# Kernel tuning notes

Measured on AMD Instinct MI355X. Metric: run time of the kernel, lower is better.

Reference implementation:

```python
import jax, jax.numpy as jnp
import numpy as np

N_STATIC, N_DYNAMIC = 64, 32
INPUT_DIM = N_STATIC + N_DYNAMIC * 9 + 8   # 360
EMBED = 64
HIDDEN = 2048
OUT = 512
T = 4096
L_IN0 = INPUT_DIM + EMBED                   # 424


def setup_inputs() -> dict:
    key = jax.random.key(0)
    ks = jax.random.split(key, 11)
    s = lambda k, shape: jax.random.normal(k, shape, jnp.float32) * 0.02
    return {
        "inputVecs": jax.random.normal(ks[0], (T, INPUT_DIM), jnp.float32),
        "Wih0": s(ks[1], (4 * HIDDEN, L_IN0)),
        "bih0": s(ks[2], (4 * HIDDEN,)),
        "bhh0": s(ks[3], (4 * HIDDEN,)),
        "Wih1": s(ks[4], (4 * HIDDEN, HIDDEN)),
        "bih1": s(ks[5], (4 * HIDDEN,)),
        "bhh1": s(ks[6], (4 * HIDDEN,)),
        "Wlin": s(ks[7], (OUT, HIDDEN)),
        "blin": s(ks[8], (OUT,)),
        "Wmap": s(ks[9], (EMBED, OUT)),
        "bmap": s(ks[10], (EMBED,)),
        "embed0": jnp.zeros((EMBED,), jnp.float32),
    }


def _cell(gates):
    # PyTorch LSTM gate order: input, forget, cell(g), output.
    # h0 = c0 = 0 each step -> c = sigmoid(i)*tanh(g), h = sigmoid(o)*tanh(c).
    i, f, g, o = jnp.split(gates, 4)
    c = jax.nn.sigmoid(i) * jnp.tanh(g)
    return jax.nn.sigmoid(o) * jnp.tanh(c)


def reference(inputVecs, Wih0, bih0, bhh0, Wih1, bih1, bhh1, Wlin, blin, Wmap, bmap, embed0):
    # The original calls nn.LSTM without hx every timestep, so PyTorch uses
    # zero initial (h, c): all W_hh @ h terms vanish; only b_hh biases remain.
    # The sole cross-time recurrence is the embed feedback loop.
    D = inputVecs.shape[1]
    Wx, We = Wih0[:, :D], Wih0[:, D:]
    # Hoist the large input GEMM out of the scan: (T, 4H)
    gates_x = inputVecs @ Wx.T + (bih0 + bhh0)
    b1 = bih1 + bhh1

    def step(embed, gx):
        h0 = _cell(gx + We @ embed)              # LSTM layer 0 (single step)
        h1 = _cell(Wih1 @ h0 + b1)               # LSTM layer 1 (single step)
        y = Wlin @ h1 + blin                     # (OUT,)  == linear(lstm_out)
        new_embed = Wmap @ jax.nn.log_softmax(y) + bmap  # map(log_softmax(y))
        return new_embed, y

    _, ys = jax.lax.scan(step, embed0, gates_x)
    return ys                                     # (T, OUT) stacked outputs
```

## Files before the change

### kernel.cpp

```cpp
#include <hip/hip_runtime.h>

#define GWG 256
#define BTH 768
#define WROW 2052
#define LDSZ 137600
#define TB   0x5AB00001

typedef float f4v __attribute__((ext_vector_type(4)));

__device__ __forceinline__ unsigned short b16(float f) {
  union { float f; unsigned int i; } z; z.f = f;
  unsigned int r = z.i + 0x7fffu + ((z.i >> 16) & 1u);
  return (unsigned short)(r >> 16);
}
__device__ __forceinline__ float bup(unsigned short u) {
  union { unsigned int i; float f; } z; z.i = ((unsigned int)u) << 16; return z.f;
}
__device__ __forceinline__ float blo(unsigned int p) {
  union { unsigned int i; float f; } z; z.i = p << 16; return z.f;
}
__device__ __forceinline__ float bhi(unsigned int p) {
  union { unsigned int i; float f; } z; z.i = p & 0xffff0000u; return z.f;
}
__device__ __forceinline__ float sigm(float x) { return 1.f / (1.f + expf(-x)); }

__device__ __forceinline__ void stG(float* p2, f4v v) {
  asm volatile("global_store_dwordx4 %0, %1, off sc0 sc1" :: "v"(p2), "v"(v) : "memory");
}

__device__ __forceinline__ void pollH(const float* mb, int tag, unsigned short* lHb) {
  const int L = threadIdx.x;
  const float* base = mb + L * 4;
  f4v v[8];
  for (;;) {
#pragma unroll
    for (int s = 0; s < 8; ++s)
      asm volatile("global_load_dwordx4 %0, %1, off sc0 sc1"
                   : "=v"(v[s]) : "v"(base + s * 256) : "memory");
    asm volatile("s_waitcnt vmcnt(0)" ::: "memory");
    __builtin_amdgcn_sched_barrier(0);
    bool ok = true;
#pragma unroll
    for (int s = 0; s < 8; ++s) ok &= (__float_as_int(v[s][3]) == tag);
    if (__all(ok)) break;
    __builtin_amdgcn_s_sleep(1);
  }
#pragma unroll
  for (int s = 0; s < 8; ++s) {
    int c = s * 64 + L;
    uint2 u; u.x = __float_as_uint(v[s][0]); u.y = __float_as_uint(v[s][1]);
    *(uint2*)&lHb[c * 4] = u;
  }
}
__device__ __forceinline__ void pollY(const float* mb, int tag, float* lY) {
  const int L = threadIdx.x;
  const float* base = mb + L * 4;
  f4v v[4];
  for (;;) {
#pragma unroll
    for (int s = 0; s < 4; ++s)
      asm volatile("global_load_dwordx4 %0, %1, off sc0 sc1"
                   : "=v"(v[s]) : "v"(base + s * 256) : "memory");
    asm volatile("s_waitcnt vmcnt(0)" ::: "memory");
    __builtin_amdgcn_sched_barrier(0);
    bool ok = true;
#pragma unroll
    for (int s = 0; s < 4; ++s) ok &= (__float_as_int(v[s][3]) == tag);
    if (__all(ok)) break;
    __builtin_amdgcn_s_sleep(1);
  }
#pragma unroll
  for (int s = 0; s < 4; ++s) {
    int c = s * 64 + L;
    lY[c * 2] = v[s][0]; lY[c * 2 + 1] = v[s][1];
  }
}

__global__ __launch_bounds__(256) void prep(const float* __restrict__ bih0, const float* __restrict__ bhh0,
                                            const float* __restrict__ bih1, const float* __restrict__ bhh1,
                                            float* __restrict__ b0, float* __restrict__ b1f) {
  int i = blockIdx.x * 256 + threadIdx.x;
  if (i < 8192) { b0[i] = bih0[i] + bhh0[i]; b1f[i] = bih1[i] + bhh1[i]; }
}

__global__ __launch_bounds__(256) void transpose_wx(const float* __restrict__ Wih0, float* __restrict__ WxT) {
  int idx = blockIdx.x * 256 + threadIdx.x;
  int r = idx & 8191, k = idx >> 13;
  WxT[(size_t)k * 8192 + r] = Wih0[(size_t)r * 424 + k];
}

__global__ __launch_bounds__(256) void gemm_gx(const float* __restrict__ inV, const float* __restrict__ WxT,
                                               const float* __restrict__ b0, unsigned short* __restrict__ gxb) {
  __shared__ float lin[32 * 360];
  int t0 = blockIdx.x * 32;
  int by = blockIdx.y;
  int ry = by >> 3;
  int gatey = ry + (ry ? 1 : 0);
  int r = gatey * 2048 + (by & 7) * 256 + threadIdx.x;
  for (int i = threadIdx.x; i < 32 * 360; i += 256) lin[i] = inV[(size_t)t0 * 360 + i];
  __syncthreads();
  float b = b0[r];
  float acc[32];
#pragma unroll
  for (int tt = 0; tt < 32; ++tt) acc[tt] = b;
  for (int k = 0; k < 360; k += 4) {
    float w0 = WxT[(size_t)(k + 0) * 8192 + r];
    float w1 = WxT[(size_t)(k + 1) * 8192 + r];
    float w2 = WxT[(size_t)(k + 2) * 8192 + r];
    float w3 = WxT[(size_t)(k + 3) * 8192 + r];
#pragma unroll
    for (int tt = 0; tt < 32; ++tt) {
      float4 l = *reinterpret_cast<const float4*>(&lin[tt * 360 + k]);
      acc[tt] = fmaf(w0, l.x, fmaf(w1, l.y, fmaf(w2, l.z, fmaf(w3, l.w, acc[tt]))));
    }
  }
  for (int tt = 0; tt < 32; ++tt) gxb[(size_t)(t0 + tt) * 8192 + r] = b16(acc[tt]);
}

__global__ __launch_bounds__(256) void wcomb_k(const float* __restrict__ Wih0, const float* __restrict__ Wmap,
                                               unsigned short* __restrict__ wcomb) {
  __shared__ float lwe[64];
  int cr = blockIdx.x;
  int orig = cr + (cr >= 2048 ? 2048 : 0);
  if (threadIdx.x < 64) lwe[threadIdx.x] = Wih0[(size_t)orig * 424 + 360 + threadIdx.x];
  __syncthreads();
  int c = threadIdx.x;
  float a0 = 0.f, a1 = 0.f;
  for (int e = 0; e < 64; ++e) {
    float w = lwe[e];
    a0 = fmaf(w, Wmap[e * 512 + c], a0);
    a1 = fmaf(w, Wmap[e * 512 + c + 256], a1);
  }
  wcomb[(size_t)cr * 512 + c] = b16(a0);
  wcomb[(size_t)cr * 512 + c + 256] = b16(a1);
}

__global__ __launch_bounds__(256) void rsk(const unsigned short* __restrict__ wcomb,
                                           const float* __restrict__ Wih0,
                                           const float* __restrict__ bmap, const float* __restrict__ emb0,
                                           float* __restrict__ rs, float* __restrict__ bcomb,
                                           float* __restrict__ g0c) {
  int cr = blockIdx.x * 256 + threadIdx.x;
  if (cr >= 6144) return;
  int orig = cr + (cr >= 2048 ? 2048 : 0);
  float s = 0.f;
  for (int k = 0; k < 512; ++k) s += bup(wcomb[(size_t)cr * 512 + k]);
  float bc = 0.f, g0 = 0.f;
  for (int e = 0; e < 64; ++e) {
    float w = Wih0[(size_t)orig * 424 + 360 + e];
    bc = fmaf(w, bmap[e], bc);
    g0 = fmaf(w, emb0[e], g0);
  }
  rs[cr] = s; bcomb[cr] = bc; g0c[cr] = g0;
}

struct KP {
  const float* Wih1; const float* Wlin; const float* blin; const float* b1f;
  const unsigned short* gxb; const unsigned short* wcomb;
  const float* rs; const float* bcomb; const float* g0c;
  float* mb_h0; float* mb_h1; float* mb_y;
  float* out;
};

__global__ __launch_bounds__(BTH) void lstm_seq(KP p) {
  extern __shared__ __align__(16) char smem[];
  unsigned short* lW1  = (unsigned short*)smem;
  unsigned short* lWcb = (unsigned short*)(smem + 98496);
  unsigned short* lWl  = (unsigned short*)(smem + 123072);
  unsigned short* lHb  = (unsigned short*)(smem + 131264);
  float* lY = (float*)(smem + 135360);
  float* lR = (float*)(smem + 137408);
  float* lV = (float*)(smem + 137504);

  const int w = blockIdx.x, tid = threadIdx.x;
  const int rl = tid >> 5;
  const int l32 = tid & 31;
  const int g3 = rl >> 3;
  const int gate = g3 + (g3 ? 1 : 0);
  const int gr  = w * 8 + (rl & 7) + 2048 * gate;
  const int crt = w * 8 + (rl & 7) + 2048 * g3;

  for (int r2 = 0; r2 < 24; ++r2) {
    int gg = r2 >> 3; int grr = w * 8 + (r2 & 7) + 2048 * (gg + (gg ? 1 : 0));
    const float* src = p.Wih1 + (size_t)grr * 2048;
    for (int i = tid; i < 2048; i += BTH) lW1[r2 * WROW + i] = b16(src[i]);
  }
  for (int i = tid; i < 24 * 512; i += BTH) {
    int r2 = i >> 9, k = i & 511;
    int crr = w * 8 + (r2 & 7) + 2048 * (r2 >> 3);
    lWcb[r2 * 512 + k] = p.wcomb[(size_t)crr * 512 + k];
  }
  for (int i = tid; i < 2 * 2048; i += BTH) {
    int q = i >> 11, k = i & 2047;
    lWl[i] = b16(p.Wlin[(size_t)(w * 2 + q) * 2048 + k]);
  }
  const float b1r = p.b1f[gr];
  const float rs_r = p.rs[crt], bc_r = p.bcomb[crt], g0_r = p.g0c[crt];
  const float bl0 = p.blin[w * 2], bl1 = p.blin[w * 2 + 1];
  unsigned short gxu = p.gxb[gr];
  __syncthreads();

  for (int t = 0; t < 4096; ++t) {
    const int tagt = TB + t;
    const unsigned short gxu_n = p.gxb[(size_t)(t < 4095 ? t + 1 : t) * 8192 + gr];
    if (t > 0) {
      if (tid < 64) pollY(p.mb_y, tagt - 1, lY);
      __syncthreads();
      float s = 0.f;
      if (tid < 512) {
        s = expf(lY[tid]);
#pragma unroll
        for (int d = 1; d < 64; d <<= 1) s += __shfl_xor(s, d);
        if ((tid & 63) == 0) lV[tid >> 6] = s;
      }
      __syncthreads();
      float lse = logf(lV[0] + lV[1] + lV[2] + lV[3] + lV[4] + lV[5] + lV[6] + lV[7]);
      float acc = 0.f;
#pragma unroll
      for (int j = 0; j < 8; ++j) {
        int k = 2 * l32 + 64 * j;
        unsigned uwp = *(const unsigned*)&lWcb[rl * 512 + k];
        float2 yv2 = *(const float2*)&lY[k];
        acc = fmaf(blo(uwp), yv2.x, fmaf(bhi(uwp), yv2.y, acc));
      }
      acc += __shfl_xor(acc, 1); acc += __shfl_xor(acc, 2); acc += __shfl_xor(acc, 4);
      acc += __shfl_xor(acc, 8); acc += __shfl_xor(acc, 16);
      if (l32 == 0) lR[rl] = bup(gxu) + acc - lse * rs_r + bc_r;
    } else {
      if (l32 == 0) lR[rl] = bup(gxu) + g0_r;
    }
    __syncthreads();
    if (tid < 8) {
      float cc = sigm(lR[tid]) * tanhf(lR[8 + tid]);
      float h  = sigm(lR[16 + tid]) * tanhf(cc);
      unsigned hb = (unsigned)b16(h);
      unsigned a0 = __shfl(hb, tid * 4 + 0);
      unsigned a1 = __shfl(hb, tid * 4 + 1);
      unsigned a2 = __shfl(hb, tid * 4 + 2);
      unsigned a3 = __shfl(hb, tid * 4 + 3);
      if (tid < 2) {
        f4v c;
        c[0] = __uint_as_float(a0 | (a1 << 16));
        c[1] = __uint_as_float(a2 | (a3 << 16));
        c[2] = 0.f; c[3] = __int_as_float(tagt);
        stG(p.mb_h0 + w * 8 + tid * 4, c);
      }
    }
    if (tid < 64) pollH(p.mb_h0, tagt, lHb);
    __syncthreads();
    {
      float acc = 0.f;
      const unsigned short* wr = lW1 + rl * WROW;
#pragma unroll 4
      for (int mm = 0; mm < 16; ++mm) {
        int k = l32 * 4 + mm * 128;
        ushort4 uw = *(const ushort4*)&wr[k];
        ushort4 uh = *(const ushort4*)&lHb[k];
        acc = fmaf(bup(uw.x), bup(uh.x), acc);
        acc = fmaf(bup(uw.y), bup(uh.y), acc);
        acc = fmaf(bup(uw.z), bup(uh.z), acc);
        acc = fmaf(bup(uw.w), bup(uh.w), acc);
      }
      acc += __shfl_xor(acc, 1); acc += __shfl_xor(acc, 2); acc += __shfl_xor(acc, 4);
      acc += __shfl_xor(acc, 8); acc += __shfl_xor(acc, 16);
      if (l32 == 0) lR[rl] = acc + b1r;
    }
    __syncthreads();
    if (tid < 8) {
      float cc = sigm(lR[tid]) * tanhf(lR[8 + tid]);
      float h  = sigm(lR[16 + tid]) * tanhf(cc);
      unsigned hb = (unsigned)b16(h);
      unsigned a0 = __shfl(hb, tid * 4 + 0);
      unsigned a1 = __shfl(hb, tid * 4 + 1);
      unsigned a2 = __shfl(hb, tid * 4 + 2);
      unsigned a3 = __shfl(hb, tid * 4 + 3);
      if (tid < 2) {
        f4v c;
        c[0] = __uint_as_float(a0 | (a1 << 16));
        c[1] = __uint_as_float(a2 | (a3 << 16));
        c[2] = 0.f; c[3] = __int_as_float(tagt);
        stG(p.mb_h1 + w * 8 + tid * 4, c);
      }
    }
    if (tid < 64) pollH(p.mb_h1, tagt, lHb);
    __syncthreads();
    if (tid < 512) {
      int q = tid >> 8, l = tid & 255;
      float a = 0.f;
#pragma unroll
      for (int it = 0; it < 2; ++it) {
        int k = it * 1024 + l * 4;
        ushort4 uw = *(const ushort4*)&lWl[q * 2048 + k];
        ushort4 uh = *(const ushort4*)&lHb[k];
        a = fmaf(bup(uw.x), bup(uh.x), a);
        a = fmaf(bup(uw.y), bup(uh.y), a);
        a = fmaf(bup(uw.z), bup(uh.z), a);
        a = fmaf(bup(uw.w), bup(uh.w), a);
      }
#pragma unroll
      for (int d = 1; d < 64; d <<= 1) a += __shfl_xor(a, d);
      if ((tid & 63) == 0) lV[tid >> 6] = a;
    }
    __syncthreads();
    if (tid == 0) {
      float y0 = lV[0] + lV[1] + lV[2] + lV[3] + bl0;
      float y1 = lV[4] + lV[5] + lV[6] + lV[7] + bl1;
      f4v c; c[0] = y0; c[1] = y1; c[2] = 0.f; c[3] = __int_as_float(tagt);
      stG(p.mb_y + w * 4, c);
      p.out[(size_t)t * 512 + w * 2]     = y0;
      p.out[(size_t)t * 512 + w * 2 + 1] = y1;
    }
    gxu = gxu_n;
  }
}

extern "C" void kernel_launch(void* const* d_in, const int* in_sizes, int n_in,
                              void* d_out, int out_size, void* d_ws, size_t ws_size,
                              hipStream_t stream) {
  const float* inV  = (const float*)d_in[0];
  const float* Wih0 = (const float*)d_in[1];
  const float* bih0 = (const float*)d_in[2];
  const float* bhh0 = (const float*)d_in[3];
  const float* Wih1 = (const float*)d_in[4];
  const float* bih1 = (const float*)d_in[5];
  const float* bhh1 = (const float*)d_in[6];
  const float* Wlin = (const float*)d_in[7];
  const float* blin = (const float*)d_in[8];
  const float* Wmap = (const float*)d_in[9];
  const float* bmap = (const float*)d_in[10];
  const float* emb0 = (const float*)d_in[11];

  char* ws = (char*)d_ws;
  unsigned short* gxb   = (unsigned short*)(ws);
  float*          WxT   = (float*)(ws + 67108864);
  unsigned short* wcomb = (unsigned short*)(ws + 67108864);
  float* b0     = (float*)(ws + 78905344);
  float* b1f    = (float*)(ws + 78938112);
  float* mb_h0  = (float*)(ws + 78970880);
  float* mb_h1  = (float*)(ws + 78979072);
  float* mb_y   = (float*)(ws + 78987264);
  float* rs     = (float*)(ws + 78991360);
  float* bcomb  = (float*)(ws + 79015936);
  float* g0c    = (float*)(ws + 79040512);
  float* out    = (float*)d_out;

  prep<<<32, 256, 0, stream>>>(bih0, bhh0, bih1, bhh1, b0, b1f);
  transpose_wx<<<11520, 256, 0, stream>>>(Wih0, WxT);
  gemm_gx<<<dim3(128, 24), 256, 0, stream>>>(inV, WxT, b0, gxb);
  wcomb_k<<<6144, 256, 0, stream>>>(Wih0, Wmap, wcomb);
  rsk<<<24, 256, 0, stream>>>(wcomb, Wih0, bmap, emb0, rs, bcomb, g0c);

  hipFuncSetAttribute(reinterpret_cast<const void*>(lstm_seq),
                      hipFuncAttributeMaxDynamicSharedMemorySize, LDSZ);
  KP p{Wih1, Wlin, blin, b1f, gxb, wcomb, rs, bcomb, g0c, mb_h0, mb_h1, mb_y, out};
  void* args[] = { (void*)&p };
  hipError_t e = hipLaunchCooperativeKernel(reinterpret_cast<void*>(&lstm_seq),
                                            dim3(GWG), dim3(BTH), args, LDSZ, stream);
  if (e != hipSuccess) {
    lstm_seq<<<GWG, BTH, LDSZ, stream>>>(p);
  }
}
```

Measured before the change: 31.46 ms.

## Fold Wmap·Wlin into layer-0 embed weights and exchange only exp-sums

Precomputes We·Wmap·Wlin (6144x2048, bf16) so the embed feedback can be computed directly from the previous h1 instead of from gathered y. Each block now publishes only the sum of exp(y) for its two outputs, so the per-step poll shrinks to a scalar log-sum-exp reduction. The h1·Wbig dot product no longer waits on the y exchange, which shortens the critical path of each step. In exchange each block reads 24 bf16 rows of 2048 from global memory every step rather than 512-wide rows from LDS. The gx buffer is also reduced to the three gates that are actually used.

```diff
diff --git a/kernel.cpp b/kernel.cpp
--- a/kernel.cpp
+++ b/kernel.cpp
@@ -3,7 +3,7 @@
 #define GWG 256
 #define BTH 768
 #define WROW 2052
-#define LDSZ 137600
+#define LDSZ 111296
 #define TB   0x5AB00001
 
 typedef float f4v __attribute__((ext_vector_type(4)));
@@ -52,7 +52,7 @@
     *(uint2*)&lHb[c * 4] = u;
   }
 }
-__device__ __forceinline__ void pollY(const float* mb, int tag, float* lY) {
+__device__ __forceinline__ void pollE(const float* mb, int tag, float* lseSlot) {
   const int L = threadIdx.x;
   const float* base = mb + L * 4;
   f4v v[4];
@@ -69,11 +69,10 @@
     if (__all(ok)) break;
     __builtin_amdgcn_s_sleep(1);
   }
-#pragma unroll
-  for (int s = 0; s < 4; ++s) {
-    int c = s * 64 + L;
-    lY[c * 2] = v[s][0]; lY[c * 2 + 1] = v[s][1];
-  }
+  float s = v[0][0] + v[1][0] + v[2][0] + v[3][0];
+#pragma unroll
+  for (int d = 1; d < 64; d <<= 1) s += __shfl_xor(s, d);
+  if (L == 0) *lseSlot = logf(s);
 }
 
 __global__ __launch_bounds__(256) void prep(const float* __restrict__ bih0, const float* __restrict__ bhh0,
@@ -96,7 +95,8 @@
   int by = blockIdx.y;
   int ry = by >> 3;
   int gatey = ry + (ry ? 1 : 0);
-  int r = gatey * 2048 + (by & 7) * 256 + threadIdx.x;
+  int r  = gatey * 2048 + (by & 7) * 256 + threadIdx.x;
+  int cr = ry    * 2048 + (by & 7) * 256 + threadIdx.x;
   for (int i = threadIdx.x; i < 32 * 360; i += 256) lin[i] = inV[(size_t)t0 * 360 + i];
   __syncthreads();
   float b = b0[r];
@@ -114,63 +114,90 @@
       acc[tt] = fmaf(w0, l.x, fmaf(w1, l.y, fmaf(w2, l.z, fmaf(w3, l.w, acc[tt]))));
     }
   }
-  for (int tt = 0; tt < 32; ++tt) gxb[(size_t)(t0 + tt) * 8192 + r] = b16(acc[tt]);
-}
-
-__global__ __launch_bounds__(256) void wcomb_k(const float* __restrict__ Wih0, const float* __restrict__ Wmap,
-                                               unsigned short* __restrict__ wcomb) {
-  __shared__ float lwe[64];
-  int cr = blockIdx.x;
-  int orig = cr + (cr >= 2048 ? 2048 : 0);
-  if (threadIdx.x < 64) lwe[threadIdx.x] = Wih0[(size_t)orig * 424 + 360 + threadIdx.x];
-  __syncthreads();
-  int c = threadIdx.x;
-  float a0 = 0.f, a1 = 0.f;
-  for (int e = 0; e < 64; ++e) {
-    float w = lwe[e];
-    a0 = fmaf(w, Wmap[e * 512 + c], a0);
-    a1 = fmaf(w, Wmap[e * 512 + c + 256], a1);
-  }
-  wcomb[(size_t)cr * 512 + c] = b16(a0);
-  wcomb[(size_t)cr * 512 + c + 256] = b16(a1);
-}
-
-__global__ __launch_bounds__(256) void rsk(const unsigned short* __restrict__ wcomb,
-                                           const float* __restrict__ Wih0,
-                                           const float* __restrict__ bmap, const float* __restrict__ emb0,
-                                           float* __restrict__ rs, float* __restrict__ bcomb,
+  for (int tt = 0; tt < 32; ++tt) gxb[(size_t)(t0 + tt) * 6144 + cr] = b16(acc[tt]);
+}
+
+__global__ __launch_bounds__(256) void wml_k(const float* __restrict__ Wmap, const float* __restrict__ Wlin,
+                                             float* __restrict__ wml) {
+  __shared__ float lm[512];
+  int e = blockIdx.x;
+  int k = blockIdx.y * 256 + threadIdx.x;
+  for (int i = threadIdx.x; i < 512; i += 256) lm[i] = Wmap[e * 512 + i];
+  __syncthreads();
+  float acc = 0.f;
+  for (int c = 0; c < 512; ++c) acc = fmaf(lm[c], Wlin[(size_t)c * 2048 + k], acc);
+  wml[(size_t)e * 2048 + k] = acc;
+}
+
+__global__ __launch_bounds__(256) void wbig_k(const float* __restrict__ Wih0, const float* __restrict__ wml,
+                                              unsigned short* __restrict__ wbig) {
+  __shared__ float lWe[32 * 64];
+  int cr0 = blockIdx.x * 32;
+  int c = blockIdx.y * 256 + threadIdx.x;
+  for (int i = threadIdx.x; i < 32 * 64; i += 256) {
+    int r2 = i >> 6, e = i & 63;
+    int cr = cr0 + r2; int orig = cr + (cr >= 2048 ? 2048 : 0);
+    lWe[i] = Wih0[(size_t)orig * 424 + 360 + e];
+  }
+  __syncthreads();
+  float wr[64];
+#pragma unroll
+  for (int e = 0; e < 64; ++e) wr[e] = wml[(size_t)e * 2048 + c];
+  for (int r2 = 0; r2 < 32; ++r2) {
+    float acc = 0.f;
+#pragma unroll
+    for (int e = 0; e < 64; ++e) acc = fmaf(lWe[r2 * 64 + e], wr[e], acc);
+    wbig[(size_t)(cr0 + r2) * 2048 + c] = b16(acc);
+  }
+}
+
+__global__ __launch_bounds__(256) void rsk(const float* __restrict__ Wih0, const float* __restrict__ Wmap,
+                                           const float* __restrict__ blin, const float* __restrict__ bmap,
+                                           const float* __restrict__ emb0,
+                                           float* __restrict__ rs, float* __restrict__ bc2,
                                            float* __restrict__ g0c) {
+  __shared__ float mrs[64], mu1[64];
+  if (threadIdx.x < 64) {
+    int e = threadIdx.x;
+    float s = 0.f, u = 0.f;
+    for (int c = 0; c < 512; ++c) {
+      float wv = Wmap[e * 512 + c];
+      s += wv; u = fmaf(wv, blin[c], u);
+    }
+    mrs[e] = s; mu1[e] = u + bmap[e];
+  }
+  __syncthreads();
   int cr = blockIdx.x * 256 + threadIdx.x;
   if (cr >= 6144) return;
   int orig = cr + (cr >= 2048 ? 2048 : 0);
-  float s = 0.f;
-  for (int k = 0; k < 512; ++k) s += bup(wcomb[(size_t)cr * 512 + k]);
-  float bc = 0.f, g0 = 0.f;
+  float a = 0.f, b = 0.f, g = 0.f;
   for (int e = 0; e < 64; ++e) {
     float w = Wih0[(size_t)orig * 424 + 360 + e];
-    bc = fmaf(w, bmap[e], bc);
-    g0 = fmaf(w, emb0[e], g0);
-  }
-  rs[cr] = s; bcomb[cr] = bc; g0c[cr] = g0;
+    a = fmaf(w, mrs[e], a);
+    b = fmaf(w, mu1[e], b);
+    g = fmaf(w, emb0[e], g);
+  }
+  rs[cr] = a; bc2[cr] = b; g0c[cr] = g;
 }
 
 struct KP {
   const float* Wih1; const float* Wlin; const float* blin; const float* b1f;
-  const unsigned short* gxb; const unsigned short* wcomb;
-  const float* rs; const float* bcomb; const float* g0c;
-  float* mb_h0; float* mb_h1; float* mb_y;
+  const unsigned short* gxb; const unsigned short* wbig;
+  const float* rs; const float* bc2; const float* g0c;
+  float* mb_h0; float* mb_h1; float* mb_e;
   float* out;
 };
 
 __global__ __launch_bounds__(BTH) void lstm_seq(KP p) {
   extern __shared__ __align__(16) char smem[];
-  unsigned short* lW1  = (unsigned short*)smem;
-  unsigned short* lWcb = (unsigned short*)(smem + 98496);
-  unsigned short* lWl  = (unsigned short*)(smem + 123072);
-  unsigned short* lHb  = (unsigned short*)(smem + 131264);
-  float* lY = (float*)(smem + 135360);
-  float* lR = (float*)(smem + 137408);
-  float* lV = (float*)(smem + 137504);
+  unsigned short* lW1 = (unsigned short*)smem;
+  unsigned short* lWl = (unsigned short*)(smem + 98496);
+  unsigned short* lHb = (unsigned short*)(smem + 106688);
+  float* lRA = (float*)(smem + 110784);
+  float* lRS = (float*)(smem + 110912);
+  float* lR  = (float*)(smem + 111040);
+  float* lV  = (float*)(smem + 111168);
+  float* lSe = (float*)(smem + 111232);
 
   const int w = blockIdx.x, tid = threadIdx.x;
   const int rl = tid >> 5;
@@ -185,54 +212,49 @@
     const float* src = p.Wih1 + (size_t)grr * 2048;
     for (int i = tid; i < 2048; i += BTH) lW1[r2 * WROW + i] = b16(src[i]);
   }
-  for (int i = tid; i < 24 * 512; i += BTH) {
-    int r2 = i >> 9, k = i & 511;
-    int crr = w * 8 + (r2 & 7) + 2048 * (r2 >> 3);
-    lWcb[r2 * 512 + k] = p.wcomb[(size_t)crr * 512 + k];
-  }
   for (int i = tid; i < 2 * 2048; i += BTH) {
     int q = i >> 11, k = i & 2047;
     lWl[i] = b16(p.Wlin[(size_t)(w * 2 + q) * 2048 + k]);
   }
-  const float b1r = p.b1f[gr];
-  const float rs_r = p.rs[crt], bc_r = p.bcomb[crt], g0_r = p.g0c[crt];
+  const float b1r  = p.b1f[gr];
+  const float rs_r = p.rs[crt], bc2_r = p.bc2[crt], g0_r = p.g0c[crt];
   const float bl0 = p.blin[w * 2], bl1 = p.blin[w * 2 + 1];
-  unsigned short gxu = p.gxb[gr];
+  unsigned short gxu = p.gxb[crt];
+  if (l32 == 0) lRS[rl] = rs_r;
+  const unsigned short* wbr = p.wbig + (size_t)crt * 2048;
   __syncthreads();
 
   for (int t = 0; t < 4096; ++t) {
     const int tagt = TB + t;
-    const unsigned short gxu_n = p.gxb[(size_t)(t < 4095 ? t + 1 : t) * 8192 + gr];
+    const unsigned short gxu_n = p.gxb[(size_t)(t < 4095 ? t + 1 : t) * 6144 + crt];
     if (t > 0) {
-      if (tid < 64) pollY(p.mb_y, tagt - 1, lY);
-      __syncthreads();
-      float s = 0.f;
-      if (tid < 512) {
-        s = expf(lY[tid]);
-#pragma unroll
-        for (int d = 1; d < 64; d <<= 1) s += __shfl_xor(s, d);
-        if ((tid & 63) == 0) lV[tid >> 6] = s;
-      }
-      __syncthreads();
-      float lse = logf(lV[0] + lV[1] + lV[2] + lV[3] + lV[4] + lV[5] + lV[6] + lV[7]);
       float acc = 0.f;
-#pragma unroll
-      for (int j = 0; j < 8; ++j) {
-        int k = 2 * l32 + 64 * j;
-        unsigned uwp = *(const unsigned*)&lWcb[rl * 512 + k];
-        float2 yv2 = *(const float2*)&lY[k];
-        acc = fmaf(blo(uwp), yv2.x, fmaf(bhi(uwp), yv2.y, acc));
+#pragma unroll 4
+      for (int mm = 0; mm < 16; ++mm) {
+        int k = l32 * 4 + mm * 128;
+        ushort4 uw = *(const ushort4*)&wbr[k];
+        ushort4 uh = *(const ushort4*)&lHb[k];
+        acc = fmaf(bup(uw.x), bup(uh.x), acc);
+        acc = fmaf(bup(uw.y), bup(uh.y), acc);
+        acc = fmaf(bup(uw.z), bup(uh.z), acc);
+        acc = fmaf(bup(uw.w), bup(uh.w), acc);
       }
       acc += __shfl_xor(acc, 1); acc += __shfl_xor(acc, 2); acc += __shfl_xor(acc, 4);
       acc += __shfl_xor(acc, 8); acc += __shfl_xor(acc, 16);
-      if (l32 == 0) lR[rl] = bup(gxu) + acc - lse * rs_r + bc_r;
+      if (l32 == 0) lRA[rl] = acc + bup(gxu) + bc2_r;
+      if (tid < 64) pollE(p.mb_e, tagt - 1, lSe);
     } else {
-      if (l32 == 0) lR[rl] = bup(gxu) + g0_r;
+      if (l32 == 0) lRA[rl] = bup(gxu) + g0_r;
+      if (tid == 0) lSe[0] = 0.f;
     }
     __syncthreads();
     if (tid < 8) {
-      float cc = sigm(lR[tid]) * tanhf(lR[8 + tid]);
-      float h  = sigm(lR[16 + tid]) * tanhf(cc);
+      float ls = lSe[0];
+      float pi = lRA[tid]      - ls * lRS[tid];
+      float pg = lRA[8 + tid]  - ls * lRS[8 + tid];
+      float po = lRA[16 + tid] - ls * lRS[16 + tid];
+      float cc = sigm(pi) * tanhf(pg);
+      float h  = sigm(po) * tanhf(cc);
       unsigned hb = (unsigned)b16(h);
       unsigned a0 = __shfl(hb, tid * 4 + 0);
       unsigned a1 = __shfl(hb, tid * 4 + 1);
@@ -305,10 +327,10 @@
     if (tid == 0) {
       float y0 = lV[0] + lV[1] + lV[2] + lV[3] + bl0;
       float y1 = lV[4] + lV[5] + lV[6] + lV[7] + bl1;
-      f4v c; c[0] = y0; c[1] = y1; c[2] = 0.f; c[3] = __int_as_float(tagt);
-      stG(p.mb_y + w * 4, c);
       p.out[(size_t)t * 512 + w * 2]     = y0;
       p.out[(size_t)t * 512 + w * 2 + 1] = y1;
+      f4v c; c[0] = expf(y0) + expf(y1); c[1] = 0.f; c[2] = 0.f; c[3] = __int_as_float(tagt);
+      stG(p.mb_e + w * 4, c);
     }
     gxu = gxu_n;
   }
@@ -331,28 +353,30 @@
   const float* emb0 = (const float*)d_in[11];
 
   char* ws = (char*)d_ws;
-  unsigned short* gxb   = (unsigned short*)(ws);
-  float*          WxT   = (float*)(ws + 67108864);
-  unsigned short* wcomb = (unsigned short*)(ws + 67108864);
-  float* b0     = (float*)(ws + 78905344);
-  float* b1f    = (float*)(ws + 78938112);
-  float* mb_h0  = (float*)(ws + 78970880);
-  float* mb_h1  = (float*)(ws + 78979072);
-  float* mb_y   = (float*)(ws + 78987264);
-  float* rs     = (float*)(ws + 78991360);
-  float* bcomb  = (float*)(ws + 79015936);
-  float* g0c    = (float*)(ws + 79040512);
-  float* out    = (float*)d_out;
+  unsigned short* gxb  = (unsigned short*)(ws);
+  float*          WxT  = (float*)(ws + 50331648);
+  unsigned short* wbig = (unsigned short*)(ws + 50331648);
+  float* wml   = (float*)(ws + 75497472);
+  float* b0    = (float*)(ws + 76021760);
+  float* b1f   = (float*)(ws + 76054528);
+  float* mb_h0 = (float*)(ws + 76087296);
+  float* mb_h1 = (float*)(ws + 76095488);
+  float* mb_e  = (float*)(ws + 76103680);
+  float* rs    = (float*)(ws + 76107776);
+  float* bc2   = (float*)(ws + 76132352);
+  float* g0c   = (float*)(ws + 76156928);
+  float* out   = (float*)d_out;
 
   prep<<<32, 256, 0, stream>>>(bih0, bhh0, bih1, bhh1, b0, b1f);
   transpose_wx<<<11520, 256, 0, stream>>>(Wih0, WxT);
   gemm_gx<<<dim3(128, 24), 256, 0, stream>>>(inV, WxT, b0, gxb);
-  wcomb_k<<<6144, 256, 0, stream>>>(Wih0, Wmap, wcomb);
-  rsk<<<24, 256, 0, stream>>>(wcomb, Wih0, bmap, emb0, rs, bcomb, g0c);
+  wml_k<<<dim3(64, 8), 256, 0, stream>>>(Wmap, Wlin, wml);
+  wbig_k<<<dim3(192, 8), 256, 0, stream>>>(Wih0, wml, wbig);
+  rsk<<<24, 256, 0, stream>>>(Wih0, Wmap, blin, bmap, emb0, rs, bc2, g0c);
 
   hipFuncSetAttribute(reinterpret_cast<const void*>(lstm_seq),
                       hipFuncAttributeMaxDynamicSharedMemorySize, LDSZ);
-  KP p{Wih1, Wlin, blin, b1f, gxb, wcomb, rs, bcomb, g0c, mb_h0, mb_h1, mb_y, out};
+  KP p{Wih1, Wlin, blin, b1f, gxb, wbig, rs, bc2, g0c, mb_h0, mb_h1, mb_e, out};
   void* args[] = { (void*)&p };
   hipError_t e = hipLaunchCooperativeKernel(reinterpret_cast<void*>(&lstm_seq),
                                             dim3(GWG), dim3(BTH), args, LDSZ, stream);
```

New measurement: 33.79 ms. 1.07x slower.

## Replicate mailbox buffers eightfold and overlap log-sum-exp with embed matvec

Applied to the files above, without the earlier changes.

Each workgroup now writes its h0, h1 and y mailbox entries to 8 replicas, and readers poll only the replica picked by blockIdx mod 8. This spreads the polling traffic of 256 workgroups over more cache lines to cut contention on the cross-workgroup sync. The log-sum-exp is now computed by a single wave from its own registers, so one barrier goes away. The lse correction is applied after the gate reduction, which lets the embed matvec run without waiting for it. The gx buffer is also compacted to only the 3 gates used, which shrinks its stride and workspace.

```diff
diff --git a/kernel.cpp b/kernel.cpp
--- a/kernel.cpp
+++ b/kernel.cpp
@@ -3,7 +3,7 @@
 #define GWG 256
 #define BTH 768
 #define WROW 2052
-#define LDSZ 137600
+#define LDSZ 137856
 #define TB   0x5AB00001
 
 typedef float f4v __attribute__((ext_vector_type(4)));
@@ -50,29 +50,6 @@
     int c = s * 64 + L;
     uint2 u; u.x = __float_as_uint(v[s][0]); u.y = __float_as_uint(v[s][1]);
     *(uint2*)&lHb[c * 4] = u;
-  }
-}
-__device__ __forceinline__ void pollY(const float* mb, int tag, float* lY) {
-  const int L = threadIdx.x;
-  const float* base = mb + L * 4;
-  f4v v[4];
-  for (;;) {
-#pragma unroll
-    for (int s = 0; s < 4; ++s)
-      asm volatile("global_load_dwordx4 %0, %1, off sc0 sc1"
-                   : "=v"(v[s]) : "v"(base + s * 256) : "memory");
-    asm volatile("s_waitcnt vmcnt(0)" ::: "memory");
-    __builtin_amdgcn_sched_barrier(0);
-    bool ok = true;
-#pragma unroll
-    for (int s = 0; s < 4; ++s) ok &= (__float_as_int(v[s][3]) == tag);
-    if (__all(ok)) break;
-    __builtin_amdgcn_s_sleep(1);
-  }
-#pragma unroll
-  for (int s = 0; s < 4; ++s) {
-    int c = s * 64 + L;
-    lY[c * 2] = v[s][0]; lY[c * 2 + 1] = v[s][1];
   }
 }
 
@@ -96,7 +73,8 @@
   int by = blockIdx.y;
   int ry = by >> 3;
   int gatey = ry + (ry ? 1 : 0);
-  int r = gatey * 2048 + (by & 7) * 256 + threadIdx.x;
+  int r  = gatey * 2048 + (by & 7) * 256 + threadIdx.x;
+  int cr = ry    * 2048 + (by & 7) * 256 + threadIdx.x;
   for (int i = threadIdx.x; i < 32 * 360; i += 256) lin[i] = inV[(size_t)t0 * 360 + i];
   __syncthreads();
   float b = b0[r];
@@ -114,7 +92,7 @@
       acc[tt] = fmaf(w0, l.x, fmaf(w1, l.y, fmaf(w2, l.z, fmaf(w3, l.w, acc[tt]))));
     }
   }
-  for (int tt = 0; tt < 32; ++tt) gxb[(size_t)(t0 + tt) * 8192 + r] = b16(acc[tt]);
+  for (int tt = 0; tt < 32; ++tt) gxb[(size_t)(t0 + tt) * 6144 + cr] = b16(acc[tt]);
 }
 
 __global__ __launch_bounds__(256) void wcomb_k(const float* __restrict__ Wih0, const float* __restrict__ Wmap,
@@ -165,12 +143,14 @@
 __global__ __launch_bounds__(BTH) void lstm_seq(KP p) {
   extern __shared__ __align__(16) char smem[];
   unsigned short* lW1  = (unsigned short*)smem;
-  unsigned short* lWcb = (unsigned short*)(smem + 98496);
-  unsigned short* lWl  = (unsigned short*)(smem + 123072);
+  unsigned short* lWl  = (unsigned short*)(smem + 98496);
+  unsigned short* lWcb = (unsigned short*)(smem + 106688);
   unsigned short* lHb  = (unsigned short*)(smem + 131264);
-  float* lY = (float*)(smem + 135360);
-  float* lR = (float*)(smem + 137408);
-  float* lV = (float*)(smem + 137504);
+  float* lY  = (float*)(smem + 135360);
+  float* lRA = (float*)(smem + 137408);
+  float* lRS = (float*)(smem + 137536);
+  float* lR  = (float*)(smem + 137664);
+  float* lV  = (float*)(smem + 137792);
 
   const int w = blockIdx.x, tid = threadIdx.x;
   const int rl = tid >> 5;
@@ -179,6 +159,7 @@
   const int gate = g3 + (g3 ? 1 : 0);
   const int gr  = w * 8 + (rl & 7) + 2048 * gate;
   const int crt = w * 8 + (rl & 7) + 2048 * g3;
+  const int rep = w & 7;
 
   for (int r2 = 0; r2 < 24; ++r2) {
     int gg = r2 >> 3; int grr = w * 8 + (r2 & 7) + 2048 * (gg + (gg ? 1 : 0));
@@ -194,27 +175,49 @@
     int q = i >> 11, k = i & 2047;
     lWl[i] = b16(p.Wlin[(size_t)(w * 2 + q) * 2048 + k]);
   }
-  const float b1r = p.b1f[gr];
+  const float b1r  = p.b1f[gr];
   const float rs_r = p.rs[crt], bc_r = p.bcomb[crt], g0_r = p.g0c[crt];
   const float bl0 = p.blin[w * 2], bl1 = p.blin[w * 2 + 1];
-  unsigned short gxu = p.gxb[gr];
+  unsigned short gxu = p.gxb[crt];
+  if (l32 == 0) lRS[rl] = rs_r;
   __syncthreads();
 
   for (int t = 0; t < 4096; ++t) {
     const int tagt = TB + t;
-    const unsigned short gxu_n = p.gxb[(size_t)(t < 4095 ? t + 1 : t) * 8192 + gr];
+    const unsigned short gxu_n = p.gxb[(size_t)(t < 4095 ? t + 1 : t) * 6144 + crt];
+    float lse = 0.f;
     if (t > 0) {
-      if (tid < 64) pollY(p.mb_y, tagt - 1, lY);
+      f4v yv[4];
+      if (tid < 64) {
+        const float* base = p.mb_y + rep * 1024 + tid * 4;
+        for (;;) {
+#pragma unroll
+          for (int s = 0; s < 4; ++s)
+            asm volatile("global_load_dwordx4 %0, %1, off sc0 sc1"
+                         : "=v"(yv[s]) : "v"(base + s * 256) : "memory");
+          asm volatile("s_waitcnt vmcnt(0)" ::: "memory");
+          __builtin_amdgcn_sched_barrier(0);
+          bool ok = true;
+#pragma unroll
+          for (int s = 0; s < 4; ++s) ok &= (__float_as_int(yv[s][3]) == tagt - 1);
+          if (__all(ok)) break;
+          __builtin_amdgcn_s_sleep(1);
+        }
+#pragma unroll
+        for (int s = 0; s < 4; ++s) {
+          int c = s * 64 + tid;
+          lY[c * 2] = yv[s][0]; lY[c * 2 + 1] = yv[s][1];
+        }
+      }
       __syncthreads();
-      float s = 0.f;
-      if (tid < 512) {
-        s = expf(lY[tid]);
+      if (tid < 64) {
+        float s = 0.f;
+#pragma unroll
+        for (int q = 0; q < 4; ++q) s += expf(yv[q][0]) + expf(yv[q][1]);
 #pragma unroll
         for (int d = 1; d < 64; d <<= 1) s += __shfl_xor(s, d);
-        if ((tid & 63) == 0) lV[tid >> 6] = s;
-      }
-      __syncthreads();
-      float lse = logf(lV[0] + lV[1] + lV[2] + lV[3] + lV[4] + lV[5] + lV[6] + lV[7]);
+        lse = logf(s);
+      }
       float acc = 0.f;
 #pragma unroll
       for (int j = 0; j < 8; ++j) {
@@ -225,28 +228,32 @@
       }
       acc += __shfl_xor(acc, 1); acc += __shfl_xor(acc, 2); acc += __shfl_xor(acc, 4);
       acc += __shfl_xor(acc, 8); acc += __shfl_xor(acc, 16);
-      if (l32 == 0) lR[rl] = bup(gxu) + acc - lse * rs_r + bc_r;
+      if (l32 == 0) lRA[rl] = bup(gxu) + acc + bc_r;
     } else {
-      if (l32 == 0) lR[rl] = bup(gxu) + g0_r;
-    }
-    __syncthreads();
-    if (tid < 8) {
-      float cc = sigm(lR[tid]) * tanhf(lR[8 + tid]);
-      float h  = sigm(lR[16 + tid]) * tanhf(cc);
-      unsigned hb = (unsigned)b16(h);
-      unsigned a0 = __shfl(hb, tid * 4 + 0);
-      unsigned a1 = __shfl(hb, tid * 4 + 1);
-      unsigned a2 = __shfl(hb, tid * 4 + 2);
-      unsigned a3 = __shfl(hb, tid * 4 + 3);
-      if (tid < 2) {
-        f4v c;
-        c[0] = __uint_as_float(a0 | (a1 << 16));
-        c[1] = __uint_as_float(a2 | (a3 << 16));
-        c[2] = 0.f; c[3] = __int_as_float(tagt);
-        stG(p.mb_h0 + w * 8 + tid * 4, c);
-      }
-    }
-    if (tid < 64) pollH(p.mb_h0, tagt, lHb);
+      if (l32 == 0) lRA[rl] = bup(gxu) + g0_r;
+    }
+    __syncthreads();
+    if (tid < 16) {
+      unsigned hb = 0u;
+      if (tid < 8) {
+        float pi = lRA[tid]      - lse * lRS[tid];
+        float pg = lRA[8 + tid]  - lse * lRS[8 + tid];
+        float po = lRA[16 + tid] - lse * lRS[16 + tid];
+        float cc = sigm(pi) * tanhf(pg);
+        hb = (unsigned)b16(sigm(po) * tanhf(cc));
+      }
+      int cpar = tid & 1;
+      unsigned a0 = __shfl(hb, cpar * 4 + 0);
+      unsigned a1 = __shfl(hb, cpar * 4 + 1);
+      unsigned a2 = __shfl(hb, cpar * 4 + 2);
+      unsigned a3 = __shfl(hb, cpar * 4 + 3);
+      f4v c;
+      c[0] = __uint_as_float(a0 | (a1 << 16));
+      c[1] = __uint_as_float(a2 | (a3 << 16));
+      c[2] = 0.f; c[3] = __int_as_float(tagt);
+      stG(p.mb_h0 + (tid >> 1) * 2048 + (w * 2 + cpar) * 4, c);
+    }
+    if (tid < 64) pollH(p.mb_h0 + rep * 2048, tagt, lHb);
     __syncthreads();
     {
       float acc = 0.f;
@@ -266,23 +273,24 @@
       if (l32 == 0) lR[rl] = acc + b1r;
     }
     __syncthreads();
-    if (tid < 8) {
-      float cc = sigm(lR[tid]) * tanhf(lR[8 + tid]);
-      float h  = sigm(lR[16 + tid]) * tanhf(cc);
-      unsigned hb = (unsigned)b16(h);
-      unsigned a0 = __shfl(hb, tid * 4 + 0);
-      unsigned a1 = __shfl(hb, tid * 4 + 1);
-      unsigned a2 = __shfl(hb, tid * 4 + 2);
-      unsigned a3 = __shfl(hb, tid * 4 + 3);
-      if (tid < 2) {
-        f4v c;
-        c[0] = __uint_as_float(a0 | (a1 << 16));
-        c[1] = __uint_as_float(a2 | (a3 << 16));
-        c[2] = 0.f; c[3] = __int_as_float(tagt);
-        stG(p.mb_h1 + w * 8 + tid * 4, c);
-      }
-    }
-    if (tid < 64) pollH(p.mb_h1, tagt, lHb);
+    if (tid < 16) {
+      unsigned hb = 0u;
+      if (tid < 8) {
+        float cc = sigm(lR[tid]) * tanhf(lR[8 + tid]);
+        hb = (unsigned)b16(sigm(lR[16 + tid]) * tanhf(cc));
+      }
+      int cpar = tid & 1;
+      unsigned a0 = __shfl(hb, cpar * 4 + 0);
+      unsigned a1 = __shfl(hb, cpar * 4 + 1);
+      unsigned a2 = __shfl(hb, cpar * 4 + 2);
+      unsigned a3 = __shfl(hb, cpar * 4 + 3);
+      f4v c;
+      c[0] = __uint_as_float(a0 | (a1 << 16));
+      c[1] = __uint_as_float(a2 | (a3 << 16));
+      c[2] = 0.f; c[3] = __int_as_float(tagt);
+      stG(p.mb_h1 + (tid >> 1) * 2048 + (w * 2 + cpar) * 4, c);
+    }
+    if (tid < 64) pollH(p.mb_h1 + rep * 2048, tagt, lHb);
     __syncthreads();
     if (tid < 512) {
       int q = tid >> 8, l = tid & 255;
@@ -302,13 +310,15 @@
       if ((tid & 63) == 0) lV[tid >> 6] = a;
     }
     __syncthreads();
-    if (tid == 0) {
+    if (tid < 8) {
       float y0 = lV[0] + lV[1] + lV[2] + lV[3] + bl0;
       float y1 = lV[4] + lV[5] + lV[6] + lV[7] + bl1;
       f4v c; c[0] = y0; c[1] = y1; c[2] = 0.f; c[3] = __int_as_float(tagt);
-      stG(p.mb_y + w * 4, c);
-      p.out[(size_t)t * 512 + w * 2]     = y0;
-      p.out[(size_t)t * 512 + w * 2 + 1] = y1;
+      stG(p.mb_y + tid * 1024 + w * 4, c);
+      if (tid == 0) {
+        p.out[(size_t)t * 512 + w * 2]     = y0;
+        p.out[(size_t)t * 512 + w * 2 + 1] = y1;
+      }
     }
     gxu = gxu_n;
   }
@@ -332,17 +342,17 @@
 
   char* ws = (char*)d_ws;
   unsigned short* gxb   = (unsigned short*)(ws);
-  float*          WxT   = (float*)(ws + 67108864);
-  unsigned short* wcomb = (unsigned short*)(ws + 67108864);
-  float* b0     = (float*)(ws + 78905344);
-  float* b1f    = (float*)(ws + 78938112);
-  float* mb_h0  = (float*)(ws + 78970880);
-  float* mb_h1  = (float*)(ws + 78979072);
-  float* mb_y   = (float*)(ws + 78987264);
-  float* rs     = (float*)(ws + 78991360);
-  float* bcomb  = (float*)(ws + 79015936);
-  float* g0c    = (float*)(ws + 79040512);
-  float* out    = (float*)d_out;
+  float*          WxT   = (float*)(ws + 50331648);
+  unsigned short* wcomb = (unsigned short*)(ws + 50331648);
+  float* b0    = (float*)(ws + 62128128);
+  float* b1f   = (float*)(ws + 62160896);
+  float* mb_h0 = (float*)(ws + 62193664);
+  float* mb_h1 = (float*)(ws + 62259200);
+  float* mb_y  = (float*)(ws + 62324736);
+  float* rs    = (float*)(ws + 62357504);
+  float* bcomb = (float*)(ws + 62382080);
+  float* g0c   = (float*)(ws + 62406656);
+  float* out   = (float*)d_out;
 
   prep<<<32, 256, 0, stream>>>(bih0, bhh0, bih1, bhh1, b0, b1f);
   transpose_wx<<<11520, 256, 0, stream>>>(Wih0, WxT);
```

Result: no change. 31.25 ms (-0.7%).
